# Performance work log

Measured on AMD Instinct MI355X. Metric: run time of the kernel, lower is better.

## Reference

```python
import jax, jax.numpy as jnp
import numpy as np

D_MODEL = 512
D_INNER = 1024   # expand=2
D_STATE = 16
D_CONV = 4
DT_RANK = 32     # ceil(d_model/16)
N_LAYERS = 3
STATE_DIM = 256
NUM_ACTIONS = 9
BATCH = 8
SEQ = 1024


def setup_inputs() -> dict:
    key = jax.random.key(0)
    ks = iter(jax.random.split(key, 32))
    def nrm(shape, scale=0.02):
        return jax.random.normal(next(ks), shape, jnp.float32) * scale
    inp = {}
    inp["state_sequences"] = jax.random.normal(next(ks), (BATCH, SEQ, STATE_DIM), jnp.float32)
    inp["embed_w"] = nrm((D_MODEL, STATE_DIM), STATE_DIM ** -0.5)
    inp["embed_b"] = jnp.zeros((D_MODEL,), jnp.float32)
    inp["in_proj_w"] = nrm((N_LAYERS, 2 * D_INNER, D_MODEL), D_MODEL ** -0.5)
    inp["conv_w"] = nrm((N_LAYERS, D_INNER, D_CONV), 0.2)
    inp["conv_b"] = jnp.zeros((N_LAYERS, D_INNER), jnp.float32)
    inp["x_proj_w"] = nrm((N_LAYERS, DT_RANK + 2 * D_STATE, D_INNER), D_INNER ** -0.5)
    inp["dt_proj_w"] = nrm((N_LAYERS, D_INNER, DT_RANK), DT_RANK ** -0.5)
    # bias so that softplus(dt) ~ 0.01 (standard mamba dt init)
    inp["dt_proj_b"] = jnp.full((N_LAYERS, D_INNER), float(np.log(np.expm1(0.01))), jnp.float32)
    # S4D-real init: A_n = n for n = 1..d_state
    inp["A_log"] = jnp.log(jnp.broadcast_to(
        jnp.arange(1, D_STATE + 1, dtype=jnp.float32), (N_LAYERS, D_INNER, D_STATE)))
    inp["D"] = jnp.ones((N_LAYERS, D_INNER), jnp.float32)
    inp["out_proj_w"] = nrm((N_LAYERS, D_MODEL, D_INNER), D_INNER ** -0.5)
    inp["head1_w"] = nrm((D_MODEL // 2, D_MODEL), D_MODEL ** -0.5)
    inp["head1_b"] = jnp.zeros((D_MODEL // 2,), jnp.float32)
    inp["head2_w"] = nrm((NUM_ACTIONS, D_MODEL // 2), (D_MODEL // 2) ** -0.5)
    inp["head2_b"] = jnp.zeros((NUM_ACTIONS,), jnp.float32)
    return inp


def _mamba_block(x, in_w, cw, cb, xw, dtw, dtb, A_log, Dp, ow):
    """One mamba-ssm Mamba layer (d_inner=2*d_model, d_state=16, d_conv=4)."""
    B, L, _ = x.shape
    xz = jnp.einsum('bld,ed->ble', x, in_w)            # (B,L,2*d_inner)
    xi, z = jnp.split(xz, 2, axis=-1)
    # causal depthwise conv1d along time
    xc = jnp.pad(xi, ((0, 0), (D_CONV - 1, 0), (0, 0)))
    conv = jax.lax.conv_general_dilated(
        xc.transpose(0, 2, 1), cw[:, None, :], (1,), 'VALID',
        feature_group_count=D_INNER)                   # (B,d_inner,L)
    xi = jax.nn.silu(conv.transpose(0, 2, 1) + cb)     # (B,L,d_inner)
    dbl = jnp.einsum('bld,ed->ble', xi, xw)            # (B,L,dt_rank+2*d_state)
    dt, Bm, Cm = jnp.split(dbl, [DT_RANK, DT_RANK + D_STATE], axis=-1)
    dt = jax.nn.softplus(jnp.einsum('blr,dr->bld', dt, dtw) + dtb)  # (B,L,d_inner)
    A = -jnp.exp(A_log)                                # (d_inner,d_state)

    def step(h, inputs):
        dt_t, x_t, B_t, C_t = inputs                   # (B,di),(B,di),(B,ds),(B,ds)
        dA = jnp.exp(dt_t[:, :, None] * A)             # (B,di,ds)
        h = dA * h + (dt_t * x_t)[:, :, None] * B_t[:, None, :]
        y_t = jnp.einsum('bds,bs->bd', h, C_t)
        return h, y_t

    h0 = jnp.zeros((B, D_INNER, D_STATE), xi.dtype)
    seq = (dt.transpose(1, 0, 2), xi.transpose(1, 0, 2),
           Bm.transpose(1, 0, 2), Cm.transpose(1, 0, 2))
    _, ys = jax.lax.scan(step, h0, seq)                # (L,B,d_inner)
    y = ys.transpose(1, 0, 2) + xi * Dp
    y = y * jax.nn.silu(z)
    return jnp.einsum('bld,ed->ble', y, ow)            # (B,L,d_model)


def reference(state_sequences, embed_w, embed_b, in_proj_w, conv_w, conv_b,
              x_proj_w, dt_proj_w, dt_proj_b, A_log, D, out_proj_w,
              head1_w, head1_b, head2_w, head2_b):
    x = jnp.einsum('bls,ds->bld', state_sequences, embed_w) + embed_b
    for i in range(N_LAYERS):
        x = _mamba_block(x, in_proj_w[i], conv_w[i], conv_b[i], x_proj_w[i],
                         dt_proj_w[i], dt_proj_b[i], A_log[i], D[i], out_proj_w[i])
    h = jax.nn.relu(jnp.einsum('bd,hd->bh', x[:, -1, :], head1_w) + head1_b)
    logits = jnp.einsum('bh,ah->ba', h, head2_w) + head2_b  # (B,num_actions)
    return logits
```

## Files before the change

kernel.cpp:

```cpp
#include <hip/hip_runtime.h>
#include <cstdint>
#include <cstddef>


#define DEVI static __device__ __forceinline__

using short8 = __attribute__((ext_vector_type(8))) short;
using f32x4  = __attribute__((ext_vector_type(4))) float;
typedef unsigned short ushort;
typedef unsigned int uint;

extern "C" __device__ float __ocml_native_exp2_f32(float);
DEVI float exp2n_(float x) { return __ocml_native_exp2_f32(x); }

DEVI float sigmoidf_(float x) { return 1.f / (1.f + __expf(-x)); }
DEVI float siluf_(float x)    { return x * sigmoidf_(x); }
DEVI float softplusf_(float x){ return fmaxf(x, 0.f) + log1pf(expf(-fabsf(x))); }

DEVI ushort rne_bf16(float f) {
    uint u = __float_as_uint(f);
    return (ushort)((u + 0x7fffu + ((u >> 16) & 1u)) >> 16);
}
DEVI float bf16_to_f(ushort h) { return __uint_as_float(((uint)h) << 16); }
DEVI uint pack_hl(float v) {
    const ushort hv = rne_bf16(v);
    const ushort lv = rne_bf16(v - bf16_to_f(hv));
    return (uint)hv | ((uint)lv << 16);
}

constexpr int LC = 32;
constexpr int NC = 32;
constexpr int PF = 4;
constexpr float LOG2E = 1.44269504f;

DEVI void cvt4(const float4 v, ushort* h, ushort* l) {
    const float vv[4] = {v.x, v.y, v.z, v.w};
    #pragma unroll
    for (int e = 0; e < 4; e++) {
        const ushort hh = rne_bf16(vv[e]);
        h[e] = hh;
        l[e] = rne_bf16(vv[e] - bf16_to_f(hh));
    }
}

__global__ __launch_bounds__(256)
void wcvt_kernel(const float* __restrict__ src, ushort* __restrict__ hi,
                 ushort* __restrict__ lo, int n4)
{
    const int idx = blockIdx.x * 256 + threadIdx.x;
    if (idx >= n4) return;
    const float4 v = reinterpret_cast<const float4*>(src)[idx];
    ushort h[4], l[4];
    cvt4(v, h, l);
    *reinterpret_cast<ushort4*>(&hi[idx * 4]) = make_ushort4(h[0], h[1], h[2], h[3]);
    *reinterpret_cast<ushort4*>(&lo[idx * 4]) = make_ushort4(l[0], l[1], l[2], l[3]);
}

__global__ __launch_bounds__(256)
void wcvt3_kernel(const float* __restrict__ s_in, const float* __restrict__ s_out,
                  const float* __restrict__ s_xp, ushort* __restrict__ dst)
{
    const int idx = blockIdx.x * 256 + threadIdx.x;
    if (idx >= 409600) return;
    const int e0 = idx * 4;
    const float* src; ushort* hb; ushort* lb; int loc;
    if (e0 < 1048576)      { src = s_in;  hb = dst;           lb = dst + 1048576; loc = e0; }
    else if (e0 < 1572864) { src = s_out; hb = dst + 2097152; lb = dst + 2621440; loc = e0 - 1048576; }
    else                   { src = s_xp;  hb = dst + 3145728; lb = dst + 3211264; loc = e0 - 1572864; }
    const float4 v = *reinterpret_cast<const float4*>(&src[loc]);
    ushort h[4], l[4];
    cvt4(v, h, l);
    *reinterpret_cast<ushort4*>(&hb[loc]) = make_ushort4(h[0], h[1], h[2], h[3]);
    *reinterpret_cast<ushort4*>(&lb[loc]) = make_ushort4(l[0], l[1], l[2], l[3]);
}

template<int ACT, int AMODE, bool OPACK>
__global__ __launch_bounds__(256)
void gemm_mfma(const float* __restrict__ A, const uint* __restrict__ Apk,
               int lda,
               const ushort* __restrict__ Whi, const ushort* __restrict__ Wlo,
               int ldw, const float* __restrict__ bias,
               float* __restrict__ C, uint* __restrict__ Cpk, int ldc, int K)
{
    __shared__ short As_hi[4096], As_lo[4096], Ws_hi[4096], Ws_lo[4096];

    const int tid  = threadIdx.x;
    const int lane = tid & 63;
    const int wave = tid >> 6;
    const int wr   = wave >> 1;
    const int wc   = wave & 1;
    const int row0 = blockIdx.y * 128;
    const int col0 = blockIdx.x * 128;

    const int g  = tid & 3;
    const int r0 = tid >> 2;

    const int lg = lane >> 4;
    const int lm = lane & 15;
    const int chA = lg * 128 + ((wr * 64 + lm) ^ lg);
    const int chB = lg * 128 + ((wc * 64 + lm) ^ lg);

    f32x4 acc[4][4];
    #pragma unroll
    for (int i = 0; i < 4; i++)
        #pragma unroll
        for (int j = 0; j < 4; j++) acc[i][j] = (f32x4){0.f, 0.f, 0.f, 0.f};

    float4 av0[2], av1[2];
    uint4  au0[2], au1[2];
    short8 wh[2], wl8[2];

    auto gload = [&](int k0) {
        #pragma unroll
        for (int p = 0; p < 2; p++) {
            const int rr = r0 + p * 64;
            if constexpr (AMODE == 1) {
                const uint* ap = Apk + (size_t)(row0 + rr) * lda + k0 + g * 8;
                au0[p] = *reinterpret_cast<const uint4*>(ap);
                au1[p] = *reinterpret_cast<const uint4*>(ap + 4);
            } else {
                const float* ap = A + (size_t)(row0 + rr) * lda + k0 + g * 8;
                av0[p] = *reinterpret_cast<const float4*>(ap);
                av1[p] = *reinterpret_cast<const float4*>(ap + 4);
            }
            const size_t wo = (size_t)(col0 + rr) * ldw + k0 + g * 8;
            wh[p]  = *reinterpret_cast<const short8*>(&Whi[wo]);
            wl8[p] = *reinterpret_cast<const short8*>(&Wlo[wo]);
        }
    };

    gload(0);

    for (int k0 = 0; k0 < K; k0 += 32) {
        #pragma unroll
        for (int p = 0; p < 2; p++) {
            const int ch = g * 128 + ((r0 + p * 64) ^ g);
            short8 h8, l8;
            if constexpr (AMODE == 1) {
                uint u[8];
                *reinterpret_cast<uint4*>(u)     = au0[p];
                *reinterpret_cast<uint4*>(u + 4) = au1[p];
                uint* hp = reinterpret_cast<uint*>(&h8);
                uint* lp = reinterpret_cast<uint*>(&l8);
                #pragma unroll
                for (int e = 0; e < 4; e++) {
                    hp[e] = __builtin_amdgcn_perm(u[2*e+1], u[2*e], 0x05040100u);
                    lp[e] = __builtin_amdgcn_perm(u[2*e+1], u[2*e], 0x07060302u);
                }
            } else {
                ushort h[8], l[8];
                cvt4(av0[p], h, l);
                cvt4(av1[p], h + 4, l + 4);
                #pragma unroll
                for (int e = 0; e < 8; e++) { h8[e] = (short)h[e]; l8[e] = (short)l[e]; }
            }
            *reinterpret_cast<short8*>(&As_hi[ch * 8]) = h8;
            *reinterpret_cast<short8*>(&As_lo[ch * 8]) = l8;
            *reinterpret_cast<short8*>(&Ws_hi[ch * 8]) = wh[p];
            *reinterpret_cast<short8*>(&Ws_lo[ch * 8]) = wl8[p];
        }
        if (k0 + 32 < K) gload(k0 + 32);
        __syncthreads();

        short8 a_hi[4], a_lo[4], b_hi[4], b_lo[4];
        #pragma unroll
        for (int i = 0; i < 4; i++) {
            a_hi[i] = *reinterpret_cast<const short8*>(&As_hi[(chA + i * 16) * 8]);
            a_lo[i] = *reinterpret_cast<const short8*>(&As_lo[(chA + i * 16) * 8]);
        }
        #pragma unroll
        for (int j = 0; j < 4; j++) {
            b_hi[j] = *reinterpret_cast<const short8*>(&Ws_hi[(chB + j * 16) * 8]);
            b_lo[j] = *reinterpret_cast<const short8*>(&Ws_lo[(chB + j * 16) * 8]);
        }
        #pragma unroll
        for (int i = 0; i < 4; i++)
            #pragma unroll
            for (int j = 0; j < 4; j++) {
                acc[i][j] = __builtin_amdgcn_mfma_f32_16x16x32_bf16(a_hi[i], b_hi[j], acc[i][j], 0, 0, 0);
                acc[i][j] = __builtin_amdgcn_mfma_f32_16x16x32_bf16(a_hi[i], b_lo[j], acc[i][j], 0, 0, 0);
                acc[i][j] = __builtin_amdgcn_mfma_f32_16x16x32_bf16(a_lo[i], b_hi[j], acc[i][j], 0, 0, 0);
            }
        __syncthreads();
    }

    #pragma unroll
    for (int i = 0; i < 4; i++) {
        const int grow = row0 + wr * 64 + i * 16 + lg * 4;
        #pragma unroll
        for (int j = 0; j < 4; j++) {
            const int gcol = col0 + wc * 64 + j * 16 + lm;
            float bv = 0.f;
            if constexpr (ACT >= 1) bv = bias[gcol];
            #pragma unroll
            for (int r = 0; r < 4; r++) {
                const float v = acc[i][j][r] + bv;
                if constexpr (OPACK) {
                    Cpk[(size_t)(grow + r) * ldc + gcol] = pack_hl(v);
                } else {
                    C[(size_t)(grow + r) * ldc + gcol] = v;
                }
            }
        }
    }
}

__global__ __launch_bounds__(256)
void gemm_mfma_xp(const float* __restrict__ A,
                  const ushort* __restrict__ Whi,
                  const ushort* __restrict__ Wlo,
                  float* __restrict__ P)
{
    __shared__ short As_hi[2048], As_lo[2048], Ws_hi[2048], Ws_lo[2048];

    const int tid  = threadIdx.x;
    const int lane = tid & 63;
    const int wave = tid >> 6;
    const int wr   = wave >> 1;
    const int wc   = wave & 1;
    const int row0 = blockIdx.x * 64;
    const int kp   = blockIdx.y;

    const int g = tid & 3;
    const int r = tid >> 2;
    const int ch_st = g * 64 + (r ^ g);

    const int lg = lane >> 4;
    const int lm = lane & 15;

    f32x4 acc[2][2];
    #pragma unroll
    for (int i = 0; i < 2; i++)
        #pragma unroll
        for (int j = 0; j < 2; j++) acc[i][j] = (f32x4){0.f, 0.f, 0.f, 0.f};

    for (int ks = 0; ks < 4; ks++) {
        const int kbase = kp * 128 + ks * 32;
        __syncthreads();
        {
            const float* ap = A + (size_t)(row0 + r) * 1024 + kbase + g * 8;
            const float4 v0 = *reinterpret_cast<const float4*>(ap);
            const float4 v1 = *reinterpret_cast<const float4*>(ap + 4);
            ushort h[8], l[8];
            cvt4(v0, h, l);
            cvt4(v1, h + 4, l + 4);
            short8 h8, l8;
            #pragma unroll
            for (int e = 0; e < 8; e++) { h8[e] = (short)h[e]; l8[e] = (short)l[e]; }
            *reinterpret_cast<short8*>(&As_hi[ch_st * 8]) = h8;
            *reinterpret_cast<short8*>(&As_lo[ch_st * 8]) = l8;
        }
        {
            const size_t wo = (size_t)r * 1024 + kbase + g * 8;
            *reinterpret_cast<short8*>(&Ws_hi[ch_st * 8]) =
                *reinterpret_cast<const short8*>(&Whi[wo]);
            *reinterpret_cast<short8*>(&Ws_lo[ch_st * 8]) =
                *reinterpret_cast<const short8*>(&Wlo[wo]);
        }
        __syncthreads();

        short8 a_hi[2], a_lo[2], b_hi[2], b_lo[2];
        #pragma unroll
        for (int i = 0; i < 2; i++) {
            const int ch = lg * 64 + ((wr * 32 + i * 16 + lm) ^ lg);
            a_hi[i] = *reinterpret_cast<const short8*>(&As_hi[ch * 8]);
            a_lo[i] = *reinterpret_cast<const short8*>(&As_lo[ch * 8]);
        }
        #pragma unroll
        for (int j = 0; j < 2; j++) {
            const int ch = lg * 64 + ((wc * 32 + j * 16 + lm) ^ lg);
            b_hi[j] = *reinterpret_cast<const short8*>(&Ws_hi[ch * 8]);
            b_lo[j] = *reinterpret_cast<const short8*>(&Ws_lo[ch * 8]);
        }
        #pragma unroll
        for (int i = 0; i < 2; i++)
            #pragma unroll
            for (int j = 0; j < 2; j++) {
                acc[i][j] = __builtin_amdgcn_mfma_f32_16x16x32_bf16(a_hi[i], b_hi[j], acc[i][j], 0, 0, 0);
                acc[i][j] = __builtin_amdgcn_mfma_f32_16x16x32_bf16(a_hi[i], b_lo[j], acc[i][j], 0, 0, 0);
                acc[i][j] = __builtin_amdgcn_mfma_f32_16x16x32_bf16(a_lo[i], b_hi[j], acc[i][j], 0, 0, 0);
            }
    }

    #pragma unroll
    for (int i = 0; i < 2; i++) {
        const int grow = row0 + wr * 32 + i * 16 + lg * 4;
        #pragma unroll
        for (int j = 0; j < 2; j++) {
            const int gcol = wc * 32 + j * 16 + lm;
            #pragma unroll
            for (int rr = 0; rr < 4; rr++)
                P[((size_t)kp * 8192 + grow + rr) * 64 + gcol] = acc[i][j][rr];
        }
    }
}

__global__ __launch_bounds__(256)
void xp_reduce(const float* __restrict__ P, float* __restrict__ dbl)
{
    const int idx = blockIdx.x * 256 + threadIdx.x;
    float s = 0.f;
    #pragma unroll
    for (int p = 0; p < 8; p++) s += P[(size_t)p * 524288 + idx];
    dbl[idx] = s;
}

__global__ __launch_bounds__(256)
void conv_silu_kernel(const float* __restrict__ xz,
                      const float* __restrict__ cw,
                      const float* __restrict__ cb,
                      float* __restrict__ xi)
{
    const int idx = blockIdx.x * 256 + threadIdx.x;
    const int d = idx & 1023;
    const int l = (idx >> 10) & 1023;
    const int b = idx >> 20;

    const float4 w = reinterpret_cast<const float4*>(cw)[d];
    float acc = cb[d];
    const float* base = xz + (size_t)b * 1024 * 2048 + d;
    if (l >= 3) acc = fmaf(base[(size_t)(l - 3) * 2048], w.x, acc);
    if (l >= 2) acc = fmaf(base[(size_t)(l - 2) * 2048], w.y, acc);
    if (l >= 1) acc = fmaf(base[(size_t)(l - 1) * 2048], w.z, acc);
    acc = fmaf(base[(size_t)l * 2048], w.w, acc);
    xi[idx] = siluf_(acc);
}

__global__ __launch_bounds__(256)
void dt_kernel(const float* __restrict__ dbl,
               const float* __restrict__ dtw,
               const float* __restrict__ dtb,
               float* __restrict__ dtout)
{
    __shared__ float S[LC][32];
    const int tid = threadIdx.x;
    const int d   = blockIdx.x * 256 + tid;
    const int c   = blockIdx.y;
    const int b   = blockIdx.z;
    const int t0  = c * LC;

    {
        const int t = tid >> 3, q = tid & 7;
        *reinterpret_cast<float4*>(&S[t][q * 4]) =
            *reinterpret_cast<const float4*>(&dbl[((size_t)b * 1024 + t0 + t) * 64 + q * 4]);
    }
    __syncthreads();

    float W[32];
    #pragma unroll
    for (int q = 0; q < 8; q++)
        *reinterpret_cast<float4*>(&W[q * 4]) =
            *reinterpret_cast<const float4*>(&dtw[(size_t)d * 32 + q * 4]);
    const float bias = dtb[d];

    float* dto = dtout + ((size_t)b * 1024 + t0) * 1024 + d;
    #pragma unroll 4
    for (int t = 0; t < LC; t++) {
        float a0 = bias, a1 = 0.f, a2 = 0.f, a3 = 0.f;
        #pragma unroll
        for (int q = 0; q < 8; q += 4) {
            const float4 s0 = *reinterpret_cast<const float4*>(&S[t][q * 4]);
            const float4 s1 = *reinterpret_cast<const float4*>(&S[t][q * 4 + 4]);
            a0 = fmaf(W[q*4+0], s0.x, a0); a1 = fmaf(W[q*4+1], s0.y, a1);
            a2 = fmaf(W[q*4+2], s0.z, a2); a3 = fmaf(W[q*4+3], s0.w, a3);
            a0 = fmaf(W[q*4+4], s1.x, a0); a1 = fmaf(W[q*4+5], s1.y, a1);
            a2 = fmaf(W[q*4+6], s1.z, a2); a3 = fmaf(W[q*4+7], s1.w, a3);
        }
        dto[(size_t)t * 1024] = softplusf_((a0 + a1) + (a2 + a3));
    }
}

__global__ __launch_bounds__(256)
void scan_p1(const float* __restrict__ xi,
             const float* __restrict__ dtin,
             const float* __restrict__ dbl,
             const float* __restrict__ A_log,
             float* __restrict__ hend,
             float* __restrict__ dtsum)
{
    __shared__ float S[LC][16];
    const int tid  = threadIdx.x;
    const int lane = tid & 63;
    const int wave = tid >> 6;
    const int dloc = lane & 31;
    const int half = lane >> 5;
    const int d    = blockIdx.x * 128 + wave * 32 + dloc;
    const int c    = blockIdx.y;
    const int b    = blockIdx.z;
    const int t0   = c * LC;

    if (tid < 128) {
        const int t = tid >> 2, q = tid & 3;
        *reinterpret_cast<float4*>(&S[t][q * 4]) =
            *reinterpret_cast<const float4*>(&dbl[((size_t)b * 1024 + t0 + t) * 64 + 32 + q * 4]);
    }
    __syncthreads();

    float A2[8], h[8];
    #pragma unroll
    for (int s = 0; s < 8; s++) {
        A2[s] = -__expf(A_log[d * 16 + half * 8 + s]) * LOG2E;
        h[s] = 0.f;
    }
    float dts = 0.f;

    const float* xi_p = xi   + ((size_t)b * 1024 + t0) * 1024 + d;
    const float* dt_p = dtin + ((size_t)b * 1024 + t0) * 1024 + d;

    float x0[PF], d0[PF], x1[PF], d1[PF], x2[PF], d2[PF];

    auto load = [&](int bt, float (&nx)[PF], float (&nd)[PF]) {
        #pragma unroll
        for (int j = 0; j < PF; j++) {
            const size_t tt = (size_t)(bt * PF + j);
            nx[j] = xi_p[tt * 1024];
            nd[j] = dt_p[tt * 1024];
        }
    };
    auto comp = [&](int bt, float (&cx)[PF], float (&cd)[PF]) {
        #pragma unroll
        for (int j = 0; j < PF; j++) {
            const int t = bt * PF + j;
            const float dtv = cd[j];
            dts += dtv;
            const float dx = dtv * cx[j];
            #pragma unroll
            for (int q = 0; q < 2; q++) {
                const float4 Bv = *reinterpret_cast<const float4*>(&S[t][half * 8 + q * 4]);
                h[q*4+0] = fmaf(exp2n_(dtv * A2[q*4+0]), h[q*4+0], dx * Bv.x);
                h[q*4+1] = fmaf(exp2n_(dtv * A2[q*4+1]), h[q*4+1], dx * Bv.y);
                h[q*4+2] = fmaf(exp2n_(dtv * A2[q*4+2]), h[q*4+2], dx * Bv.z);
                h[q*4+3] = fmaf(exp2n_(dtv * A2[q*4+3]), h[q*4+3], dx * Bv.w);
            }
        }
    };

    load(0, x0, d0); load(1, x1, d1);
    load(2, x2, d2); comp(0, x0, d0);
    load(3, x0, d0); comp(1, x1, d1);
    load(4, x1, d1); comp(2, x2, d2);
    load(5, x2, d2); comp(3, x0, d0);
    load(6, x0, d0); comp(4, x1, d1);
    load(7, x1, d1); comp(5, x2, d2);
    comp(6, x0, d0);
    comp(7, x1, d1);

    float* hp = hend + (((size_t)b * NC + c) * 1024 + d) * 16 + half * 8;
    *reinterpret_cast<float4*>(&hp[0]) = *reinterpret_cast<const float4*>(&h[0]);
    *reinterpret_cast<float4*>(&hp[4]) = *reinterpret_cast<const float4*>(&h[4]);
    if (half == 0) dtsum[((size_t)b * NC + c) * 1024 + d] = dts;
}

__global__ __launch_bounds__(256)
void scan_p2(float* __restrict__ hbuf,
             const float* __restrict__ dtsum,
             const float* __restrict__ A_log)
{
    const int gid = blockIdx.x * 256 + threadIdx.x;
    const int s = gid & 15;
    const int d = (gid >> 4) & 1023;
    const int b = gid >> 14;

    const float A2 = -__expf(A_log[d * 16 + s]) * LOG2E;
    float h = 0.f;
    #pragma unroll
    for (int c = 0; c < NC; c++) {
        const size_t idx = (((size_t)b * NC + c) * 1024 + d) * 16 + s;
        const float he = hbuf[idx];
        const float aP = exp2n_(A2 * dtsum[((size_t)b * NC + c) * 1024 + d]);
        hbuf[idx] = h;
        h = fmaf(aP, h, he);
    }
}

__global__ __launch_bounds__(256)
void scan_p3(const float* __restrict__ xi,
             const float* __restrict__ dtin,
             const float* __restrict__ dbl,
             float* __restrict__ xz,
             const float* __restrict__ A_log,
             const float* __restrict__ Dp,
             const float* __restrict__ h0)
{
    __shared__ float S[LC][32];
    const int tid  = threadIdx.x;
    const int lane = tid & 63;
    const int wave = tid >> 6;
    const int dloc = lane & 31;
    const int half = lane >> 5;
    const int d    = blockIdx.x * 128 + wave * 32 + dloc;
    const int c    = blockIdx.y;
    const int b    = blockIdx.z;
    const int t0   = c * LC;

    {
        const int t = tid >> 3, q = tid & 7;
        *reinterpret_cast<float4*>(&S[t][q * 4]) =
            *reinterpret_cast<const float4*>(&dbl[((size_t)b * 1024 + t0 + t) * 64 + 32 + q * 4]);
    }
    __syncthreads();

    float A2[8], h[8];
    #pragma unroll
    for (int s = 0; s < 8; s++)
        A2[s] = -__expf(A_log[d * 16 + half * 8 + s]) * LOG2E;
    const float* h0p = h0 + (((size_t)b * NC + c) * 1024 + d) * 16 + half * 8;
    *reinterpret_cast<float4*>(&h[0]) = *reinterpret_cast<const float4*>(&h0p[0]);
    *reinterpret_cast<float4*>(&h[4]) = *reinterpret_cast<const float4*>(&h0p[4]);

    const float Dv = Dp[d];
    const float* xi_p = xi   + ((size_t)b * 1024 + t0) * 1024 + d;
    const float* dt_p = dtin + ((size_t)b * 1024 + t0) * 1024 + d;
    const float* z_p  = xz   + ((size_t)b * 1024 + t0) * 2048 + 1024 + d;
    uint* ypk_p = reinterpret_cast<uint*>(xz) + ((size_t)b * 1024 + t0) * 2048 + d;

    float x0[PF], z0[PF], d0[PF], x1[PF], z1[PF], d1[PF], x2[PF], z2[PF], d2[PF];

    auto load = [&](int bt, float (&nx)[PF], float (&nz)[PF], float (&nd)[PF]) {
        #pragma unroll
        for (int j = 0; j < PF; j++) {
            const size_t tt = (size_t)(bt * PF + j);
            nx[j] = xi_p[tt * 1024];
            nz[j] = z_p[tt * 2048];
            nd[j] = dt_p[tt * 1024];
        }
    };
    auto comp = [&](int bt, float (&cx)[PF], float (&cz)[PF], float (&cd)[PF]) {
        #pragma unroll
        for (int j = 0; j < PF; j++) {
            const int t = bt * PF + j;
            const float dtv = cd[j];
            const float dx  = dtv * cx[j];
            float y = 0.f;
            #pragma unroll
            for (int q = 0; q < 2; q++) {
                const float4 Bv = *reinterpret_cast<const float4*>(&S[t][half * 8 + q * 4]);
                const float4 Cv = *reinterpret_cast<const float4*>(&S[t][16 + half * 8 + q * 4]);
                h[q*4+0] = fmaf(exp2n_(dtv * A2[q*4+0]), h[q*4+0], dx * Bv.x);
                h[q*4+1] = fmaf(exp2n_(dtv * A2[q*4+1]), h[q*4+1], dx * Bv.y);
                h[q*4+2] = fmaf(exp2n_(dtv * A2[q*4+2]), h[q*4+2], dx * Bv.z);
                h[q*4+3] = fmaf(exp2n_(dtv * A2[q*4+3]), h[q*4+3], dx * Bv.w);
                y = fmaf(h[q*4+0], Cv.x, y);
                y = fmaf(h[q*4+1], Cv.y, y);
                y = fmaf(h[q*4+2], Cv.z, y);
                y = fmaf(h[q*4+3], Cv.w, y);
            }
            const float yfull = y + __shfl_xor(y, 32);
            if (half == 0) {
                const float yv = (yfull + cx[j] * Dv) * siluf_(cz[j]);
                ypk_p[(size_t)t * 2048] = pack_hl(yv);
            }
        }
    };

    load(0, x0, z0, d0); load(1, x1, z1, d1);
    load(2, x2, z2, d2); comp(0, x0, z0, d0);
    load(3, x0, z0, d0); comp(1, x1, z1, d1);
    load(4, x1, z1, d1); comp(2, x2, z2, d2);
    load(5, x2, z2, d2); comp(3, x0, z0, d0);
    load(6, x0, z0, d0); comp(4, x1, z1, d1);
    load(7, x1, z1, d1); comp(5, x2, z2, d2);
    comp(6, x0, z0, d0);
    comp(7, x1, z1, d1);
}

__global__ __launch_bounds__(256)
void head1_kernel(const uint* __restrict__ xpk,
                  const float* __restrict__ w,
                  const float* __restrict__ bias,
                  float* __restrict__ hh)
{
    const int tid = threadIdx.x;
    const int jl  = tid >> 4;
    const int ks  = tid & 15;
    const int j   = blockIdx.x * 16 + jl;

    const float* wr = w + (size_t)j * 512 + ks * 32;
    float acc[8];
    #pragma unroll
    for (int b = 0; b < 8; b++) {
        const size_t ro = ((size_t)b * 1024 + 1023) * 512 + ks * 32;
        float a = 0.f;
        #pragma unroll
        for (int k = 0; k < 32; k += 4) {
            const float4 wv = *reinterpret_cast<const float4*>(&wr[k]);
            const uint4  pv = *reinterpret_cast<const uint4*>(&xpk[ro + k]);
            a = fmaf(wv.x, bf16_to_f((ushort)(pv.x & 0xffff)) + bf16_to_f((ushort)(pv.x >> 16)), a);
            a = fmaf(wv.y, bf16_to_f((ushort)(pv.y & 0xffff)) + bf16_to_f((ushort)(pv.y >> 16)), a);
            a = fmaf(wv.z, bf16_to_f((ushort)(pv.z & 0xffff)) + bf16_to_f((ushort)(pv.z >> 16)), a);
            a = fmaf(wv.w, bf16_to_f((ushort)(pv.w & 0xffff)) + bf16_to_f((ushort)(pv.w >> 16)), a);
        }
        acc[b] = a;
    }
    #pragma unroll
    for (int b = 0; b < 8; b++) {
        float p = acc[b];
        p += __shfl_xor(p, 1);
        p += __shfl_xor(p, 2);
        p += __shfl_xor(p, 4);
        p += __shfl_xor(p, 8);
        if (ks == 0) hh[b * 256 + j] = fmaxf(p + bias[j], 0.f);
    }
}

__global__ void head2_kernel(const float* __restrict__ hh,
                             const float* __restrict__ w,
                             const float* __restrict__ b2,
                             float* __restrict__ out)
{
    const int t = threadIdx.x;
    if (t < 72) {
        const int bb = t / 9, a = t % 9;
        const float* hr = hh + bb * 256;
        const float* wr = w + a * 256;
        float acc = b2[a];
        for (int jj = 0; jj < 256; jj++) acc = fmaf(hr[jj], wr[jj], acc);
        out[t] = acc;
    }
}


extern "C" void kernel_launch(void* const* d_in, const int* in_sizes, int n_in,
                              void* d_out, int out_size, void* d_ws, size_t ws_size,
                              hipStream_t stream)
{
    const float* state     = (const float*)d_in[0];
    const float* embed_w   = (const float*)d_in[1];
    const float* embed_b   = (const float*)d_in[2];
    const float* in_proj_w = (const float*)d_in[3];
    const float* conv_w    = (const float*)d_in[4];
    const float* conv_b    = (const float*)d_in[5];
    const float* x_proj_w  = (const float*)d_in[6];
    const float* dt_proj_w = (const float*)d_in[7];
    const float* dt_proj_b = (const float*)d_in[8];
    const float* A_log     = (const float*)d_in[9];
    const float* Dp        = (const float*)d_in[10];
    const float* out_proj_w= (const float*)d_in[11];
    const float* h1w       = (const float*)d_in[12];
    const float* h1b       = (const float*)d_in[13];
    const float* h2w       = (const float*)d_in[14];
    const float* h2b       = (const float*)d_in[15];
    float* out = (float*)d_out;

    float* reg0 = (float*)d_ws;
    uint*  xpk  = (uint*)reg0;
    float* dblp = reg0;
    float* hbuf = reg0;

    float* xz   = reg0 + (size_t)8192 * 512;
    float* xi   = xz   + (size_t)8192 * 2048;
    float* dtbf = xi   + (size_t)8192 * 1024;
    float* dbl  = dtbf + (size_t)8192 * 1024;
    float* hh   = dbl  + (size_t)8192 * 64;
    ushort* wl = (ushort*)(hh + 2048);
    ushort* we_hi = wl + 3276800;
    ushort* we_lo = we_hi + 131072;
    float* dtsum = (float*)(we_lo + 131072);

    uint* ypk = (uint*)xz;

    const dim3 blk(256);

    wcvt_kernel<<<dim3(128), blk, 0, stream>>>(embed_w, we_hi, we_lo, 131072 / 4);
    gemm_mfma<1, 0, true><<<dim3(4, 64), blk, 0, stream>>>(
        state, nullptr, 256, we_hi, we_lo, 256, embed_b,
        nullptr, xpk, 512, 256);

    for (int i = 0; i < 3; i++) {
        const float* Alog_i = A_log + (size_t)i * 1024 * 16;
        const float* dtw_i  = dt_proj_w + (size_t)i * 1024 * 32;
        const float* dtb_i  = dt_proj_b + (size_t)i * 1024;

        wcvt3_kernel<<<dim3(1600), blk, 0, stream>>>(
            in_proj_w + (size_t)i * 2048 * 512,
            out_proj_w + (size_t)i * 512 * 1024,
            x_proj_w + (size_t)i * 64 * 1024, wl);

        gemm_mfma<0, 1, false><<<dim3(16, 64), blk, 0, stream>>>(
            nullptr, xpk, 512, wl, wl + 1048576, 512, nullptr,
            xz, nullptr, 2048, 512);

        conv_silu_kernel<<<dim3(8 * 1024 * 1024 / 256), blk, 0, stream>>>(
            xz, conv_w + (size_t)i * 1024 * 4, conv_b + (size_t)i * 1024, xi);

        gemm_mfma_xp<<<dim3(128, 8), blk, 0, stream>>>(
            xi, wl + 3145728, wl + 3211264, dblp);
        xp_reduce<<<dim3(2048), blk, 0, stream>>>(dblp, dbl);

        dt_kernel<<<dim3(4, NC, 8), blk, 0, stream>>>(dbl, dtw_i, dtb_i, dtbf);

        scan_p1<<<dim3(8, NC, 8), blk, 0, stream>>>(
            xi, dtbf, dbl, Alog_i, hbuf, dtsum);
        scan_p2<<<dim3(512), blk, 0, stream>>>(hbuf, dtsum, Alog_i);
        scan_p3<<<dim3(8, NC, 8), blk, 0, stream>>>(
            xi, dtbf, dbl, xz, Alog_i, Dp + (size_t)i * 1024, hbuf);

        gemm_mfma<0, 1, true><<<dim3(4, 64), blk, 0, stream>>>(
            nullptr, ypk, 2048, wl + 2097152, wl + 2621440, 1024, nullptr,
            nullptr, xpk, 512, 1024);
    }

    head1_kernel<<<dim3(16), blk, 0, stream>>>(xpk, h1w, h1b, hh);
    head2_kernel<<<dim3(1), dim3(128), 0, stream>>>(hh, h2w, h2b, out);
}
```

Measured before the change: 789.9 us.

## Split in_proj output into separate x and z buffers and swizzle GEMM block order

The in_proj GEMM now writes its x half and z half into two contiguous 1024-wide buffers instead of one interleaved 2048-wide buffer. This shortens the row strides read by conv and scan_p3, and scan_p3 writes its packed y output in place over the dt buffer. A block-index swizzle is also added to both GEMM kernels so that consecutive workgroups spread across tiles, aiming at better cache or XCD locality. The aliasing of y over dt depends on each element of dt being read before it is overwritten within the same thread.

```diff
diff --git a/kernel.cpp b/kernel.cpp
--- a/kernel.cpp
+++ b/kernel.cpp
@@ -26,6 +26,15 @@
     const ushort hv = rne_bf16(v);
     const ushort lv = rne_bf16(v - bf16_to_f(hv));
     return (uint)hv | ((uint)lv << 16);
+}
+
+DEVI void swz_block(int& bx, int& by, int gx, int gy) {
+    const int total = gx * gy;
+    const int q = total >> 3;
+    const int id = by * gx + bx;
+    const int s = (id & 7) * q + (id >> 3);
+    bx = s % gx;
+    by = s / gx;
 }
 
 constexpr int LC = 32;
@@ -80,17 +89,21 @@
                int lda,
                const ushort* __restrict__ Whi, const ushort* __restrict__ Wlo,
                int ldw, const float* __restrict__ bias,
-               float* __restrict__ C, uint* __restrict__ Cpk, int ldc, int K)
+               float* C, float* C2, int nsplit,
+               uint* __restrict__ Cpk, int ldc, int K)
 {
     __shared__ short As_hi[4096], As_lo[4096], Ws_hi[4096], Ws_lo[4096];
+
+    int bx = blockIdx.x, by = blockIdx.y;
+    swz_block(bx, by, gridDim.x, gridDim.y);
 
     const int tid  = threadIdx.x;
     const int lane = tid & 63;
     const int wave = tid >> 6;
     const int wr   = wave >> 1;
     const int wc   = wave & 1;
-    const int row0 = blockIdx.y * 128;
-    const int col0 = blockIdx.x * 128;
+    const int row0 = by * 128;
+    const int col0 = bx * 128;
 
     const int g  = tid & 3;
     const int r0 = tid >> 2;
@@ -184,6 +197,10 @@
         __syncthreads();
     }
 
+    float* Cw = C;
+    int cofs = 0;
+    if (C2 != nullptr && col0 >= nsplit) { Cw = C2; cofs = nsplit; }
+
     #pragma unroll
     for (int i = 0; i < 4; i++) {
         const int grow = row0 + wr * 64 + i * 16 + lg * 4;
@@ -198,7 +215,7 @@
                 if constexpr (OPACK) {
                     Cpk[(size_t)(grow + r) * ldc + gcol] = pack_hl(v);
                 } else {
-                    C[(size_t)(grow + r) * ldc + gcol] = v;
+                    Cw[(size_t)(grow + r) * ldc + (gcol - cofs)] = v;
                 }
             }
         }
@@ -212,14 +229,17 @@
                   float* __restrict__ P)
 {
     __shared__ short As_hi[2048], As_lo[2048], Ws_hi[2048], Ws_lo[2048];
+
+    int bx = blockIdx.x, by = blockIdx.y;
+    swz_block(bx, by, gridDim.x, gridDim.y);
 
     const int tid  = threadIdx.x;
     const int lane = tid & 63;
     const int wave = tid >> 6;
     const int wr   = wave >> 1;
     const int wc   = wave & 1;
-    const int row0 = blockIdx.x * 64;
-    const int kp   = blockIdx.y;
+    const int row0 = bx * 64;
+    const int kp   = by;
 
     const int g = tid & 3;
     const int r = tid >> 2;
@@ -306,7 +326,7 @@
 }
 
 __global__ __launch_bounds__(256)
-void conv_silu_kernel(const float* __restrict__ xz,
+void conv_silu_kernel(const float* __restrict__ xpre,
                       const float* __restrict__ cw,
                       const float* __restrict__ cb,
                       float* __restrict__ xi)
@@ -318,11 +338,11 @@
 
     const float4 w = reinterpret_cast<const float4*>(cw)[d];
     float acc = cb[d];
-    const float* base = xz + (size_t)b * 1024 * 2048 + d;
-    if (l >= 3) acc = fmaf(base[(size_t)(l - 3) * 2048], w.x, acc);
-    if (l >= 2) acc = fmaf(base[(size_t)(l - 2) * 2048], w.y, acc);
-    if (l >= 1) acc = fmaf(base[(size_t)(l - 1) * 2048], w.z, acc);
-    acc = fmaf(base[(size_t)l * 2048], w.w, acc);
+    const float* base = xpre + (size_t)b * 1024 * 1024 + d;
+    if (l >= 3) acc = fmaf(base[(size_t)(l - 3) * 1024], w.x, acc);
+    if (l >= 2) acc = fmaf(base[(size_t)(l - 2) * 1024], w.y, acc);
+    if (l >= 1) acc = fmaf(base[(size_t)(l - 1) * 1024], w.z, acc);
+    acc = fmaf(base[(size_t)l * 1024], w.w, acc);
     xi[idx] = siluf_(acc);
 }
 
@@ -475,9 +495,9 @@
 
 __global__ __launch_bounds__(256)
 void scan_p3(const float* __restrict__ xi,
-             const float* __restrict__ dtin,
+             float* dtio,
              const float* __restrict__ dbl,
-             float* __restrict__ xz,
+             const float* __restrict__ zbuf,
              const float* __restrict__ A_log,
              const float* __restrict__ Dp,
              const float* __restrict__ h0)
@@ -509,10 +529,11 @@
     *reinterpret_cast<float4*>(&h[4]) = *reinterpret_cast<const float4*>(&h0p[4]);
 
     const float Dv = Dp[d];
-    const float* xi_p = xi   + ((size_t)b * 1024 + t0) * 1024 + d;
-    const float* dt_p = dtin + ((size_t)b * 1024 + t0) * 1024 + d;
-    const float* z_p  = xz   + ((size_t)b * 1024 + t0) * 2048 + 1024 + d;
-    uint* ypk_p = reinterpret_cast<uint*>(xz) + ((size_t)b * 1024 + t0) * 2048 + d;
+    const size_t rowbase = ((size_t)b * 1024 + t0) * 1024 + d;
+    const float* xi_p = xi + rowbase;
+    const float* dt_p = dtio + rowbase;
+    const float* z_p  = zbuf + rowbase;
+    uint* ypk_p = reinterpret_cast<uint*>(dtio) + rowbase;
 
     float x0[PF], z0[PF], d0[PF], x1[PF], z1[PF], d1[PF], x2[PF], z2[PF], d2[PF];
 
@@ -521,7 +542,7 @@
         for (int j = 0; j < PF; j++) {
             const size_t tt = (size_t)(bt * PF + j);
             nx[j] = xi_p[tt * 1024];
-            nz[j] = z_p[tt * 2048];
+            nz[j] = z_p[tt * 1024];
             nd[j] = dt_p[tt * 1024];
         }
     };
@@ -548,7 +569,7 @@
             const float yfull = y + __shfl_xor(y, 32);
             if (half == 0) {
                 const float yv = (yfull + cx[j] * Dv) * siluf_(cz[j]);
-                ypk_p[(size_t)t * 2048] = pack_hl(yv);
+                ypk_p[(size_t)t * 1024] = pack_hl(yv);
             }
         }
     };
@@ -647,8 +668,9 @@
     float* dblp = reg0;
     float* hbuf = reg0;
 
-    float* xz   = reg0 + (size_t)8192 * 512;
-    float* xi   = xz   + (size_t)8192 * 2048;
+    float* xpre = reg0 + (size_t)8192 * 512;
+    float* zbuf = xpre + (size_t)8192 * 1024;
+    float* xi   = zbuf + (size_t)8192 * 1024;
     float* dtbf = xi   + (size_t)8192 * 1024;
     float* dbl  = dtbf + (size_t)8192 * 1024;
     float* hh   = dbl  + (size_t)8192 * 64;
@@ -657,14 +679,14 @@
     ushort* we_lo = we_hi + 131072;
     float* dtsum = (float*)(we_lo + 131072);
 
-    uint* ypk = (uint*)xz;
+    uint* ypk = (uint*)dtbf;
 
     const dim3 blk(256);
 
     wcvt_kernel<<<dim3(128), blk, 0, stream>>>(embed_w, we_hi, we_lo, 131072 / 4);
     gemm_mfma<1, 0, true><<<dim3(4, 64), blk, 0, stream>>>(
         state, nullptr, 256, we_hi, we_lo, 256, embed_b,
-        nullptr, xpk, 512, 256);
+        nullptr, nullptr, 0, xpk, 512, 256);
 
     for (int i = 0; i < 3; i++) {
         const float* Alog_i = A_log + (size_t)i * 1024 * 16;
@@ -678,10 +700,10 @@
 
         gemm_mfma<0, 1, false><<<dim3(16, 64), blk, 0, stream>>>(
             nullptr, xpk, 512, wl, wl + 1048576, 512, nullptr,
-            xz, nullptr, 2048, 512);
+            xpre, zbuf, 1024, nullptr, 1024, 512);
 
         conv_silu_kernel<<<dim3(8 * 1024 * 1024 / 256), blk, 0, stream>>>(
-            xz, conv_w + (size_t)i * 1024 * 4, conv_b + (size_t)i * 1024, xi);
+            xpre, conv_w + (size_t)i * 1024 * 4, conv_b + (size_t)i * 1024, xi);
 
         gemm_mfma_xp<<<dim3(128, 8), blk, 0, stream>>>(
             xi, wl + 3145728, wl + 3211264, dblp);
@@ -693,11 +715,11 @@
             xi, dtbf, dbl, Alog_i, hbuf, dtsum);
         scan_p2<<<dim3(512), blk, 0, stream>>>(hbuf, dtsum, Alog_i);
         scan_p3<<<dim3(8, NC, 8), blk, 0, stream>>>(
-            xi, dtbf, dbl, xz, Alog_i, Dp + (size_t)i * 1024, hbuf);
+            xi, dtbf, dbl, zbuf, Alog_i, Dp + (size_t)i * 1024, hbuf);
 
         gemm_mfma<0, 1, true><<<dim3(4, 64), blk, 0, stream>>>(
-            nullptr, ypk, 2048, wl + 2097152, wl + 2621440, 1024, nullptr,
-            nullptr, xpk, 512, 1024);
+            nullptr, ypk, 1024, wl + 2097152, wl + 2621440, 1024, nullptr,
+            nullptr, nullptr, 0, xpk, 512, 1024);
     }
 
     head1_kernel<<<dim3(16), blk, 0, stream>>>(xpk, h1w, h1b, hh);
```

New measurement: 766.1 us. 3.0% less time.
